# Optimization experiments

Measured on AMD Instinct MI355X. Metric: run time of the kernel, lower is better.

## Reference

```python
import jax, jax.numpy as jnp
import numpy as np

RADII = np.array([0.5, 1.0, 1.5, 2.0], dtype=np.float32)
SIGMA = 0.5          # gaussian radial-function width (= radius spacing)
EPS = 1e-8
N_SH = 9             # real spherical harmonics up to l=2
N_BASIS = len(RADII) * N_SH


def real_sh_l2(u):
    """Real spherical harmonics l=0,1,2 of unit vectors u[..., 3] -> [..., 9]."""
    x, y, z = u[..., 0], u[..., 1], u[..., 2]
    one = jnp.ones_like(x)
    return jnp.stack([
        0.28209479 * one,
        0.48860251 * x, 0.48860251 * y, 0.48860251 * z,
        1.09254843 * x * y,
        1.09254843 * y * z,
        0.31539157 * (3.0 * z * z - 1.0),
        1.09254843 * x * z,
        0.54627421 * (x * x - y * y),
    ], axis=-1)


def setup_inputs() -> dict:
    key = jax.random.key(0)
    k1, k2, k3, k4, k5 = jax.random.split(key, 5)
    n, c_in, d_out, b, a = 4, 32, 32, 8192, 32
    inp = jax.random.normal(k1, (n, c_in, b), jnp.float32)
    coords = jax.random.uniform(k2, (n, b, 3), jnp.float32) * 4.0
    neighbors = jax.random.randint(k3, (n, b, a), 0, b)
    relative_mask = jax.random.uniform(k4, (n, b, a), jnp.float32)
    W = jax.random.normal(k5, (d_out, c_in, N_BASIS), jnp.float32) / np.sqrt(c_in * N_BASIS)
    return {"input": inp, "coords": coords, "relative_mask": relative_mask,
            "W": W, "neighbors": neighbors}


def reference(input, coords, relative_mask, W, neighbors):
    n, c, b = input.shape
    idx_n = jnp.arange(n)[:, None, None]                     # [n,1,1]
    # neighbor difference matrix: coords[neighbors] - coords  -> [n,b,a,3]
    neigh_xyz = coords[idx_n, neighbors]
    diff = neigh_xyz - coords[:, :, None, :]
    r = jnp.linalg.norm(diff, axis=-1)                       # [n,b,a]
    u = diff / (r[..., None] + EPS)
    Y = real_sh_l2(u)                                        # [n,b,a,9]
    radii = jnp.asarray(RADII)
    rb = jnp.exp(-((r[..., None] - radii) / SIGMA) ** 2)     # [n,b,a,4]
    basis = (rb[..., :, None] * Y[..., None, :]).reshape(r.shape + (-1,))  # [n,b,a,36]
    # neighbor feature matrix: input[n, :, neighbors[n,b,a]] -> [n,b,a,c]
    feat = input[idx_n, :, neighbors]
    # relative_mask multiplies k over (n,b,a) == masking gathered features
    feat = feat * relative_mask[..., None]
    # fused form of: k[d,c,n,b,a] = sum_k basis[n,b,a,k] W[d,c,k];
    # out[n,d,b] = sum_{c,a} feat[n,b,a,c] * k[d,c,n,b,a]
    M = jnp.einsum('nbac,nbak->nbck', feat, basis)           # [n,b,c,36]
    return jnp.einsum('nbck,dck->ndb', M, W)
```

## Files before the change

kernel.cpp:

```cpp
#include <hip/hip_runtime.h>
#include <hip/hip_bf16.h>


typedef _Float16 f16x8 __attribute__((ext_vector_type(8)));
typedef _Float16 f16x4 __attribute__((ext_vector_type(4)));
typedef __fp16   h16x2 __attribute__((ext_vector_type(2)));
typedef float    f32x4 __attribute__((ext_vector_type(4)));
typedef unsigned int u32;

__device__ __forceinline__ u32 pk16(float a, float b) {
    union { h16x2 v; u32 u; } cv;
    cv.v = __builtin_amdgcn_cvt_pkrtz(a, b);
    return cv.u;
}
__device__ __forceinline__ unsigned short f16bits(float v) {
    const _Float16 hv = (_Float16)v;
    return __builtin_bit_cast(unsigned short, hv);
}

__device__ __forceinline__ void geom(float dx, float dy, float dz, float msk, int h_,
                                     float Y[9], float& rbA, float& rbB) {
    const float r   = sqrtf(dx * dx + dy * dy + dz * dz);
    const float inv = 1.0f / (r + 1e-8f);
    const float x = dx * inv, y = dy * inv, z = dz * inv;
    Y[0] = 0.28209479f;
    Y[1] = 0.48860251f * x;
    Y[2] = 0.48860251f * y;
    Y[3] = 0.48860251f * z;
    Y[4] = 1.09254843f * x * y;
    Y[5] = 1.09254843f * y * z;
    Y[6] = 0.31539157f * (3.0f * z * z - 1.0f);
    Y[7] = 1.09254843f * x * z;
    Y[8] = 0.54627421f * (x * x - y * y);
    const float t0 = (r - 0.5f) * 2.0f;
    const float t1 = (r - 1.0f) * 2.0f;
    const float t2 = (r - 1.5f) * 2.0f;
    const float t3 = (r - 2.0f) * 2.0f;
    const float rb0 = __expf(-t0 * t0) * msk;
    const float rb1 = __expf(-t1 * t1) * msk;
    const float rb2 = __expf(-t2 * t2) * msk;
    const float rb3 = __expf(-t3 * t3) * msk;
    rbA = h_ ? rb2 : rb0;
    rbB = h_ ? rb3 : rb1;
}

__global__ __launch_bounds__(256) void prep_kernel(
    const float* __restrict__ inp, const float* __restrict__ W,
    float* __restrict__ inp_t, unsigned short* __restrict__ Wfrag)
{
    if (blockIdx.x < 1024) {
        __shared__ float T[32][33];
        const int n  = blockIdx.x >> 8;
        const int b0 = (blockIdx.x & 255) << 5;
        const int bx = threadIdx.x & 31;
        const int cy = threadIdx.x >> 5;
        #pragma unroll
        for (int r = 0; r < 4; ++r) {
            const int cc = cy + r * 8;
            T[bx][cc] = inp[((n << 5) + cc) * 8192 + b0 + bx];
        }
        __syncthreads();
        #pragma unroll
        for (int r = 0; r < 4; ++r) {
            const int by = cy + r * 8;
            inp_t[((n << 13) + b0 + by) * 32 + bx] = T[by][bx];
        }
    } else {
        const int t = (blockIdx.x - 1024) * 256 + threadIdx.x;
        if (t < 36 * 2 * 64 * 8) {
            const int j  = t & 7;
            const int l  = (t >> 3) & 63;
            const int dt = (t >> 9) & 1;
            const int kt = t >> 10;
            const int d  = dt * 16 + (l & 15);
            const int c  = ((l >> 4) << 3) + j;
            Wfrag[t] = f16bits(W[d * 1152 + c * 36 + kt]);
        }
    }
}

__global__ __launch_bounds__(512, 4) void se3_main(
    const float* __restrict__ inp_t, const float* __restrict__ coords,
    const float* __restrict__ rmask, const int* __restrict__ neigh,
    const unsigned short* __restrict__ Wfrag, float* __restrict__ out)
{
    __shared__ __align__(16) unsigned short Mb_s[36 * 580];
    __shared__ __align__(16) unsigned short bas[8][37 * 36];
    __shared__ int idxs[16][32];
    __shared__ __align__(16) float Cp[8 * 64 * 4];

    const int tid  = threadIdx.x;
    const int lane = tid & 63;
    const int w    = tid >> 6;
    const int l15  = lane & 15;
    const int q    = lane >> 4;
    const int a_   = lane & 31;
    const int h_   = lane >> 5;

    const int blk = blockIdx.x;
    const int n_  = (blk & 7) >> 1;
    const int pos = ((blk >> 3) << 1) | (blk & 1);
    const int b0  = pos << 4;
    const int gp0 = (n_ << 13) | b0;
    const int nbase_pt = n_ << 13;
    const float* __restrict__ inp_n = inp_t + ((size_t)n_ << 18);

    unsigned short* basw = &bas[w][0];

    const int ph0 = 2 * l15;
    const int ph1 = (l15 < 2) ? (32 + 2 * l15) : (2 * l15 - 3);
    const int ph2 = (l15 < 4) ? (29 + 2 * l15) : 36;
    const int offB0 = ph0 * 36 + (q << 3);
    const int offB1 = ph1 * 36 + (q << 3);
    const int offB2 = ph2 * 36 + (q << 3);

    const int pA = w << 1, pB = pA | 1;
    const int gpA = gp0 + pA, gpB = gp0 + pB;

    const int   idxA = neigh[(gpA << 5) | a_];
    const int   idxB = neigh[(gpB << 5) | a_];
    const float mskA = rmask[(gpA << 5) | a_];
    const float mskB = rmask[(gpB << 5) | a_];
    const float cxA = coords[gpA * 3 + 0], cyA = coords[gpA * 3 + 1], czA = coords[gpA * 3 + 2];
    const float cxB = coords[gpB * 3 + 0], cyB = coords[gpB * 3 + 1], czB = coords[gpB * 3 + 2];
    if (lane < 32) { idxs[pA][a_] = idxA; idxs[pB][a_] = idxB; }
    const int nbA = (nbase_pt + idxA) * 3;
    const int nbB = (nbase_pt + idxB) * 3;
    const float dxA = coords[nbA + 0] - cxA, dyA = coords[nbA + 1] - cyA, dzA = coords[nbA + 2] - czA;
    const float dxB = coords[nbB + 0] - cxB, dyB = coords[nbB + 1] - cyB, dzB = coords[nbB + 2] - czB;

    float fA0[8], fA1[8], fB0[8], fB1[8];
    #pragma unroll
    for (int j = 0; j < 8; ++j) {
        const int ri = idxs[pA][(q << 3) + j];
        const float* rp = inp_n + (((unsigned)ri) << 5) + l15;
        fA0[j] = rp[0]; fA1[j] = rp[16];
    }
    #pragma unroll
    for (int j = 0; j < 8; ++j) {
        const int ri = idxs[pB][(q << 3) + j];
        const float* rp = inp_n + (((unsigned)ri) << 5) + l15;
        fB0[j] = rp[0]; fB1[j] = rp[16];
    }

    float YA[9], YB[9], rbA_A, rbB_A, rbA_B, rbB_B;
    geom(dxA, dyA, dzA, mskA, h_, YA, rbA_A, rbB_A);
    geom(dxB, dyB, dzB, mskB, h_, YB, rbA_B, rbB_B);

    #pragma unroll
    for (int t = 0; t < 18; ++t) {
        const float v = (t < 9) ? rbA_A * YA[t] : rbB_A * YA[t - 9];
        basw[(2 * t + h_) * 36 + a_] = f16bits(v);
    }

    f16x4 blo, bhi;
    blo = *(const f16x4*)&basw[offB0]; bhi = *(const f16x4*)&basw[offB0 + 4];
    const f16x8 BfA0 = __builtin_shufflevector(blo, bhi, 0, 1, 2, 3, 4, 5, 6, 7);
    blo = *(const f16x4*)&basw[offB1]; bhi = *(const f16x4*)&basw[offB1 + 4];
    const f16x8 BfA1 = __builtin_shufflevector(blo, bhi, 0, 1, 2, 3, 4, 5, 6, 7);
    blo = *(const f16x4*)&basw[offB2]; bhi = *(const f16x4*)&basw[offB2 + 4];
    const f16x8 BfA2 = __builtin_shufflevector(blo, bhi, 0, 1, 2, 3, 4, 5, 6, 7);

    union { f16x8 v; u32 u[4]; } afA0, afA1, afB0, afB1;
    #pragma unroll
    for (int j4 = 0; j4 < 4; ++j4) {
        afA0.u[j4] = pk16(fA0[2 * j4], fA0[2 * j4 + 1]);
        afA1.u[j4] = pk16(fA1[2 * j4], fA1[2 * j4 + 1]);
    }
    const f32x4 z4 = {0.0f, 0.0f, 0.0f, 0.0f};
    f32x4 DA00 = __builtin_amdgcn_mfma_f32_16x16x32_f16(afA0.v, BfA0, z4, 0, 0, 0);
    f32x4 DA01 = __builtin_amdgcn_mfma_f32_16x16x32_f16(afA0.v, BfA1, z4, 0, 0, 0);
    f32x4 DA02 = __builtin_amdgcn_mfma_f32_16x16x32_f16(afA0.v, BfA2, z4, 0, 0, 0);
    f32x4 DA10 = __builtin_amdgcn_mfma_f32_16x16x32_f16(afA1.v, BfA0, z4, 0, 0, 0);
    f32x4 DA11 = __builtin_amdgcn_mfma_f32_16x16x32_f16(afA1.v, BfA1, z4, 0, 0, 0);
    f32x4 DA12 = __builtin_amdgcn_mfma_f32_16x16x32_f16(afA1.v, BfA2, z4, 0, 0, 0);

    #pragma unroll
    for (int t = 0; t < 18; ++t) {
        const float v = (t < 9) ? rbA_B * YB[t] : rbB_B * YB[t - 9];
        basw[(2 * t + h_) * 36 + a_] = f16bits(v);
    }
    blo = *(const f16x4*)&basw[offB0]; bhi = *(const f16x4*)&basw[offB0 + 4];
    const f16x8 BfB0 = __builtin_shufflevector(blo, bhi, 0, 1, 2, 3, 4, 5, 6, 7);
    blo = *(const f16x4*)&basw[offB1]; bhi = *(const f16x4*)&basw[offB1 + 4];
    const f16x8 BfB1 = __builtin_shufflevector(blo, bhi, 0, 1, 2, 3, 4, 5, 6, 7);
    blo = *(const f16x4*)&basw[offB2]; bhi = *(const f16x4*)&basw[offB2 + 4];
    const f16x8 BfB2 = __builtin_shufflevector(blo, bhi, 0, 1, 2, 3, 4, 5, 6, 7);

    #pragma unroll
    for (int j4 = 0; j4 < 4; ++j4) {
        afB0.u[j4] = pk16(fB0[2 * j4], fB0[2 * j4 + 1]);
        afB1.u[j4] = pk16(fB1[2 * j4], fB1[2 * j4 + 1]);
    }
    f32x4 DB00 = __builtin_amdgcn_mfma_f32_16x16x32_f16(afB0.v, BfB0, z4, 0, 0, 0);
    f32x4 DB01 = __builtin_amdgcn_mfma_f32_16x16x32_f16(afB0.v, BfB1, z4, 0, 0, 0);
    f32x4 DB02 = __builtin_amdgcn_mfma_f32_16x16x32_f16(afB0.v, BfB2, z4, 0, 0, 0);
    f32x4 DB10 = __builtin_amdgcn_mfma_f32_16x16x32_f16(afB1.v, BfB0, z4, 0, 0, 0);
    f32x4 DB11 = __builtin_amdgcn_mfma_f32_16x16x32_f16(afB1.v, BfB1, z4, 0, 0, 0);
    f32x4 DB12 = __builtin_amdgcn_mfma_f32_16x16x32_f16(afB1.v, BfB2, z4, 0, 0, 0);

    {
        const int rowpA = pA * 36 + (q << 2);
        const int a0 = l15 * 580 + rowpA;
        const int a1 = (16 + l15) * 580 + rowpA;
        *(u32*)&Mb_s[a0]      = pk16(DA00[0], DA00[1]);
        *(u32*)&Mb_s[a0 + 2]  = pk16(DA00[2], DA00[3]);
        *(u32*)&Mb_s[a0 + 16] = pk16(DA10[0], DA10[1]);
        *(u32*)&Mb_s[a0 + 18] = pk16(DA10[2], DA10[3]);
        *(u32*)&Mb_s[a1]      = pk16(DA01[0], DA01[1]);
        *(u32*)&Mb_s[a1 + 2]  = pk16(DA01[2], DA01[3]);
        *(u32*)&Mb_s[a1 + 16] = pk16(DA11[0], DA11[1]);
        *(u32*)&Mb_s[a1 + 18] = pk16(DA11[2], DA11[3]);
        const int rowpB = pB * 36 + (q << 2);
        const int c0 = l15 * 580 + rowpB;
        const int c1 = (16 + l15) * 580 + rowpB;
        *(u32*)&Mb_s[c0]      = pk16(DB00[0], DB00[1]);
        *(u32*)&Mb_s[c0 + 2]  = pk16(DB00[2], DB00[3]);
        *(u32*)&Mb_s[c0 + 16] = pk16(DB10[0], DB10[1]);
        *(u32*)&Mb_s[c0 + 18] = pk16(DB10[2], DB10[3]);
        *(u32*)&Mb_s[c1]      = pk16(DB01[0], DB01[1]);
        *(u32*)&Mb_s[c1 + 2]  = pk16(DB01[2], DB01[3]);
        *(u32*)&Mb_s[c1 + 16] = pk16(DB11[0], DB11[1]);
        *(u32*)&Mb_s[c1 + 18] = pk16(DB11[2], DB11[3]);
        if (l15 < 4) {
            const int a2 = (32 + l15) * 580 + rowpA;
            *(u32*)&Mb_s[a2]      = pk16(DA02[0], DA02[1]);
            *(u32*)&Mb_s[a2 + 2]  = pk16(DA02[2], DA02[3]);
            *(u32*)&Mb_s[a2 + 16] = pk16(DA12[0], DA12[1]);
            *(u32*)&Mb_s[a2 + 18] = pk16(DA12[2], DA12[3]);
            const int c2 = (32 + l15) * 580 + rowpB;
            *(u32*)&Mb_s[c2]      = pk16(DB02[0], DB02[1]);
            *(u32*)&Mb_s[c2 + 2]  = pk16(DB02[2], DB02[3]);
            *(u32*)&Mb_s[c2 + 16] = pk16(DB12[0], DB12[1]);
            *(u32*)&Mb_s[c2 + 18] = pk16(DB12[2], DB12[3]);
        }
    }
    __syncthreads();

    {
        const int dt  = w >> 2;
        const int seg = w & 3;
        f32x4 acc2 = {0.0f, 0.0f, 0.0f, 0.0f};
        const int kt0 = seg * 9;
        #pragma unroll 3
        for (int kt = kt0; kt < kt0 + 9; ++kt) {
            const f16x8 af = *(const f16x8*)&Wfrag[((size_t)((kt * 2 + dt) * 64 + lane)) << 3];
            const int mbase = kt * 580 + l15 * 36 + (q << 3);
            const f16x4 mlo = *(const f16x4*)&Mb_s[mbase];
            const f16x4 mhi = *(const f16x4*)&Mb_s[mbase + 4];
            const f16x8 bf  = __builtin_shufflevector(mlo, mhi, 0, 1, 2, 3, 4, 5, 6, 7);
            acc2 = __builtin_amdgcn_mfma_f32_16x16x32_f16(af, bf, acc2, 0, 0, 0);
        }
        *(f32x4*)&Cp[(w * 64 + lane) * 4] = acc2;
    }
    __syncthreads();

    if (w < 2) {
        const int dt2 = w;
        f32x4 s = *(const f32x4*)&Cp[((dt2 * 4 + 0) * 64 + lane) * 4];
        #pragma unroll
        for (int rphase = 1; rphase < 4; ++rphase) {
            const f32x4 t = *(const f32x4*)&Cp[((dt2 * 4 + rphase) * 64 + lane) * 4];
            s[0] += t[0]; s[1] += t[1]; s[2] += t[2]; s[3] += t[3];
        }
        const int drow = dt2 * 16 + (lane >> 4) * 4;
        const int col  = b0 + (lane & 15);
        #pragma unroll
        for (int rr = 0; rr < 4; ++rr) {
            out[(((n_ << 5) + drow + rr) << 13) + col] = s[rr];
        }
    }
}

extern "C" void kernel_launch(void* const* d_in, const int* in_sizes, int n_in,
                              void* d_out, int out_size, void* d_ws, size_t ws_size,
                              hipStream_t stream)
{
    const float* inp    = (const float*)d_in[0];
    const float* coords = (const float*)d_in[1];
    const float* rmask  = (const float*)d_in[2];
    const float* W      = (const float*)d_in[3];
    const int*   neigh  = (const int*)d_in[4];
    float*       outp   = (float*)d_out;

    float*          inp_t = (float*)d_ws;
    unsigned short* Wfrag = (unsigned short*)((char*)d_ws + (4u << 20));

    prep_kernel<<<1168, 256, 0, stream>>>(inp, W, inp_t, Wfrag);
    se3_main<<<2048, 512, 0, stream>>>(inp_t, coords, rmask, neigh, Wfrag, outp);
}
```

Before: 93.04 us.

## Store transposed input as fp16 and pad basis LDS stride

The prep kernel now writes the transposed input features as fp16 instead of fp32. This halves the bytes fetched by the random neighbor gathers in the main kernel and removes the per-element pack conversion before the MFMA. It also pads the per-wave basis LDS row stride from 36 to 44 to reduce bank conflicts, and stores neighbor indices in LDS as 16-bit values. Precision is unchanged in effect, since the values were already rounded to fp16 before the MFMA, though the rounding mode changes from round-toward-zero to round-to-nearest.

```diff
diff --git a/kernel.cpp b/kernel.cpp
--- a/kernel.cpp
+++ b/kernel.cpp
@@ -17,6 +17,8 @@
     const _Float16 hv = (_Float16)v;
     return __builtin_bit_cast(unsigned short, hv);
 }
+
+#define BAS_STRIDE 44
 
 __device__ __forceinline__ void geom(float dx, float dy, float dz, float msk, int h_,
                                      float Y[9], float& rbA, float& rbB) {
@@ -46,7 +48,7 @@
 
 __global__ __launch_bounds__(256) void prep_kernel(
     const float* __restrict__ inp, const float* __restrict__ W,
-    float* __restrict__ inp_t, unsigned short* __restrict__ Wfrag)
+    unsigned short* __restrict__ inp_t16, unsigned short* __restrict__ Wfrag)
 {
     if (blockIdx.x < 1024) {
         __shared__ float T[32][33];
@@ -63,7 +65,7 @@
         #pragma unroll
         for (int r = 0; r < 4; ++r) {
             const int by = cy + r * 8;
-            inp_t[((n << 13) + b0 + by) * 32 + bx] = T[by][bx];
+            inp_t16[((n << 13) + b0 + by) * 32 + bx] = f16bits(T[by][bx]);
         }
     } else {
         const int t = (blockIdx.x - 1024) * 256 + threadIdx.x;
@@ -80,13 +82,13 @@
 }
 
 __global__ __launch_bounds__(512, 4) void se3_main(
-    const float* __restrict__ inp_t, const float* __restrict__ coords,
+    const unsigned short* __restrict__ inp_t16, const float* __restrict__ coords,
     const float* __restrict__ rmask, const int* __restrict__ neigh,
     const unsigned short* __restrict__ Wfrag, float* __restrict__ out)
 {
     __shared__ __align__(16) unsigned short Mb_s[36 * 580];
-    __shared__ __align__(16) unsigned short bas[8][37 * 36];
-    __shared__ int idxs[16][32];
+    __shared__ __align__(16) unsigned short bas[8][37 * BAS_STRIDE];
+    __shared__ unsigned short idxs[16][32];
     __shared__ __align__(16) float Cp[8 * 64 * 4];
 
     const int tid  = threadIdx.x;
@@ -103,16 +105,16 @@
     const int b0  = pos << 4;
     const int gp0 = (n_ << 13) | b0;
     const int nbase_pt = n_ << 13;
-    const float* __restrict__ inp_n = inp_t + ((size_t)n_ << 18);
+    const unsigned short* __restrict__ inp_n = inp_t16 + ((size_t)n_ << 18);
 
     unsigned short* basw = &bas[w][0];
 
     const int ph0 = 2 * l15;
     const int ph1 = (l15 < 2) ? (32 + 2 * l15) : (2 * l15 - 3);
     const int ph2 = (l15 < 4) ? (29 + 2 * l15) : 36;
-    const int offB0 = ph0 * 36 + (q << 3);
-    const int offB1 = ph1 * 36 + (q << 3);
-    const int offB2 = ph2 * 36 + (q << 3);
+    const int offB0 = ph0 * BAS_STRIDE + (q << 3);
+    const int offB1 = ph1 * BAS_STRIDE + (q << 3);
+    const int offB2 = ph2 * BAS_STRIDE + (q << 3);
 
     const int pA = w << 1, pB = pA | 1;
     const int gpA = gp0 + pA, gpB = gp0 + pB;
@@ -123,24 +125,29 @@
     const float mskB = rmask[(gpB << 5) | a_];
     const float cxA = coords[gpA * 3 + 0], cyA = coords[gpA * 3 + 1], czA = coords[gpA * 3 + 2];
     const float cxB = coords[gpB * 3 + 0], cyB = coords[gpB * 3 + 1], czB = coords[gpB * 3 + 2];
-    if (lane < 32) { idxs[pA][a_] = idxA; idxs[pB][a_] = idxB; }
+    if (lane < 32) {
+        idxs[pA][a_] = (unsigned short)idxA;
+        idxs[pB][a_] = (unsigned short)idxB;
+    }
     const int nbA = (nbase_pt + idxA) * 3;
     const int nbB = (nbase_pt + idxB) * 3;
     const float dxA = coords[nbA + 0] - cxA, dyA = coords[nbA + 1] - cyA, dzA = coords[nbA + 2] - czA;
     const float dxB = coords[nbB + 0] - cxB, dyB = coords[nbB + 1] - cyB, dzB = coords[nbB + 2] - czB;
 
-    float fA0[8], fA1[8], fB0[8], fB1[8];
+    u32 fA0[8], fA1[8], fB0[8], fB1[8];
     #pragma unroll
     for (int j = 0; j < 8; ++j) {
         const int ri = idxs[pA][(q << 3) + j];
-        const float* rp = inp_n + (((unsigned)ri) << 5) + l15;
-        fA0[j] = rp[0]; fA1[j] = rp[16];
+        const unsigned short* rp = inp_n + (((unsigned)ri) << 5) + l15;
+        fA0[j] = rp[0];
+        fA1[j] = rp[16];
     }
     #pragma unroll
     for (int j = 0; j < 8; ++j) {
         const int ri = idxs[pB][(q << 3) + j];
-        const float* rp = inp_n + (((unsigned)ri) << 5) + l15;
-        fB0[j] = rp[0]; fB1[j] = rp[16];
+        const unsigned short* rp = inp_n + (((unsigned)ri) << 5) + l15;
+        fB0[j] = rp[0];
+        fB1[j] = rp[16];
     }
 
     float YA[9], YB[9], rbA_A, rbB_A, rbA_B, rbB_B;
@@ -150,7 +157,7 @@
     #pragma unroll
     for (int t = 0; t < 18; ++t) {
         const float v = (t < 9) ? rbA_A * YA[t] : rbB_A * YA[t - 9];
-        basw[(2 * t + h_) * 36 + a_] = f16bits(v);
+        basw[(2 * t + h_) * BAS_STRIDE + a_] = f16bits(v);
     }
 
     f16x4 blo, bhi;
@@ -164,8 +171,8 @@
     union { f16x8 v; u32 u[4]; } afA0, afA1, afB0, afB1;
     #pragma unroll
     for (int j4 = 0; j4 < 4; ++j4) {
-        afA0.u[j4] = pk16(fA0[2 * j4], fA0[2 * j4 + 1]);
-        afA1.u[j4] = pk16(fA1[2 * j4], fA1[2 * j4 + 1]);
+        afA0.u[j4] = fA0[2 * j4] | (fA0[2 * j4 + 1] << 16);
+        afA1.u[j4] = fA1[2 * j4] | (fA1[2 * j4 + 1] << 16);
     }
     const f32x4 z4 = {0.0f, 0.0f, 0.0f, 0.0f};
     f32x4 DA00 = __builtin_amdgcn_mfma_f32_16x16x32_f16(afA0.v, BfA0, z4, 0, 0, 0);
@@ -178,7 +185,7 @@
     #pragma unroll
     for (int t = 0; t < 18; ++t) {
         const float v = (t < 9) ? rbA_B * YB[t] : rbB_B * YB[t - 9];
-        basw[(2 * t + h_) * 36 + a_] = f16bits(v);
+        basw[(2 * t + h_) * BAS_STRIDE + a_] = f16bits(v);
     }
     blo = *(const f16x4*)&basw[offB0]; bhi = *(const f16x4*)&basw[offB0 + 4];
     const f16x8 BfB0 = __builtin_shufflevector(blo, bhi, 0, 1, 2, 3, 4, 5, 6, 7);
@@ -189,8 +196,8 @@
 
     #pragma unroll
     for (int j4 = 0; j4 < 4; ++j4) {
-        afB0.u[j4] = pk16(fB0[2 * j4], fB0[2 * j4 + 1]);
-        afB1.u[j4] = pk16(fB1[2 * j4], fB1[2 * j4 + 1]);
+        afB0.u[j4] = fB0[2 * j4] | (fB0[2 * j4 + 1] << 16);
+        afB1.u[j4] = fB1[2 * j4] | (fB1[2 * j4 + 1] << 16);
     }
     f32x4 DB00 = __builtin_amdgcn_mfma_f32_16x16x32_f16(afB0.v, BfB0, z4, 0, 0, 0);
     f32x4 DB01 = __builtin_amdgcn_mfma_f32_16x16x32_f16(afB0.v, BfB1, z4, 0, 0, 0);
@@ -283,9 +290,9 @@
     const int*   neigh  = (const int*)d_in[4];
     float*       outp   = (float*)d_out;
 
-    float*          inp_t = (float*)d_ws;
-    unsigned short* Wfrag = (unsigned short*)((char*)d_ws + (4u << 20));
-
-    prep_kernel<<<1168, 256, 0, stream>>>(inp, W, inp_t, Wfrag);
-    se3_main<<<2048, 512, 0, stream>>>(inp_t, coords, rmask, neigh, Wfrag, outp);
-}
+    unsigned short* inp_t16 = (unsigned short*)d_ws;
+    unsigned short* Wfrag   = (unsigned short*)((char*)d_ws + (2u << 20));
+
+    prep_kernel<<<1168, 256, 0, stream>>>(inp, W, inp_t16, Wfrag);
+    se3_main<<<2048, 512, 0, stream>>>(inp_t16, coords, rmask, neigh, Wfrag, outp);
+}
```

Measured after the change: 92.91 us. No clear change (-0.1%).
